# Kernel tuning notes

Measured on AMD Instinct MI355X. Metric: run time of the kernel, lower is better.

The kernel has to match this reference:

```python
import jax, jax.numpy as jnp
import numpy as np

B, T, D = 1, 1024, 2048
F_DIM = 1408
E = 8
TOPK = 2


def setup_inputs() -> dict:
    key = jax.random.key(0)
    ks = jax.random.split(key, 5)
    x = jax.random.normal(ks[0], (B, T, D), dtype=jnp.float32)
    # torch nn.Linear weight layout: [out_features, in_features]
    gate_w = jax.random.normal(ks[1], (E, D), dtype=jnp.float32) * 0.02
    gate_proj = jax.random.normal(ks[2], (E, F_DIM, D), dtype=jnp.float32) * 0.02
    up_proj = jax.random.normal(ks[3], (E, F_DIM, D), dtype=jnp.float32) * 0.02
    down_proj = jax.random.normal(ks[4], (E, D, F_DIM), dtype=jnp.float32) * 0.02
    return {"x": x, "gate_w": gate_w, "gate_proj": gate_proj,
            "up_proj": up_proj, "down_proj": down_proj}


def reference(x, gate_w, gate_proj, up_proj, down_proj):
    b, t, d = x.shape
    x_flat = x.reshape(-1, d)                                  # [N, D]
    n = x_flat.shape[0]
    # Router: top-k logits then softmax over the selected k.
    router_logits = x_flat @ gate_w.T                          # [N, E]
    top_w, sel = jax.lax.top_k(router_logits, TOPK)            # [N, K]
    top_w = jax.nn.softmax(top_w, axis=-1)                     # [N, K]
    # Scatter routing weights into dense per-token expert weights [N, E].
    tok_ids = jnp.arange(n)[:, None]
    tw = jnp.zeros((n, E), dtype=x.dtype).at[tok_ids, sel].add(top_w)
    # Dense expert compute (mathematically identical: unselected experts get
    # zero combine weight). SwiGLU per expert.
    g = jnp.einsum('nd,efd->enf', x_flat, gate_proj)           # [E, N, F]
    u = jnp.einsum('nd,efd->enf', x_flat, up_proj)             # [E, N, F]
    h = jax.nn.silu(g) * u                                     # [E, N, F]
    eo = jnp.einsum('enf,edf->end', h, down_proj)              # [E, N, D]
    out = jnp.einsum('end,ne->nd', eo, tw)                     # [N, D]
    return out.reshape(b, t, d)
```

## Files before the change

kernel.cpp:

```cpp
#include <hip/hip_runtime.h>
#include <hip/hip_bf16.h>
#include <stdint.h>

typedef __attribute__((ext_vector_type(8))) short short8;
typedef __attribute__((ext_vector_type(4))) float f32x4;
typedef unsigned int u32;
typedef unsigned short u16;

static constexpr int N_TOK = 1024;
static constexpr int DDIM = 2048;
static constexpr int FDIM = 1408;
static constexpr int NEXP = 8;
static constexpr int MAXROWS = 3072;
static constexpr int NT128 = 24;

static constexpr size_t O_META   = 0;
static constexpr size_t O_TE128  = 256;
static constexpr size_t O_TR128  = 384;
static constexpr size_t O_ROWTOK = 768;
static constexpr size_t O_TOKROWS= O_ROWTOK + (size_t)MAXROWS * 4;
static constexpr size_t O_SEL    = O_TOKROWS + 2048 * 4;
static constexpr size_t O_W      = O_SEL + 2048 * 4;
static constexpr size_t O_XBF    = (O_W + 2048 * 4 + 255) & ~(size_t)255;
static constexpr size_t O_H      = O_XBF + (size_t)(N_TOK + 1) * DDIM * 2;
static constexpr size_t O_EO     = O_H + (size_t)MAXROWS * FDIM * 2;

static __device__ __forceinline__ u16 f2bf(float f) {
    return __builtin_bit_cast(u16, __float2bfloat16(f));
}
static __device__ __forceinline__ float bf2f(u16 s) {
    u32 u = ((u32)s) << 16;
    return __builtin_bit_cast(float, u);
}
static __device__ __forceinline__ u32 pack2(float a, float b) {
    return (u32)f2bf(a) | ((u32)f2bf(b) << 16);
}
static __device__ __forceinline__ void gload16(const void* g, void* l) {
    __builtin_amdgcn_global_load_lds(
        (const __attribute__((address_space(1))) void*)g,
        (__attribute__((address_space(3))) void*)l, 16, 0, 0);
}
#define PIN() __builtin_amdgcn_sched_barrier(0)
static __device__ __forceinline__ void sync_lgkm() {
    asm volatile("s_waitcnt lgkmcnt(0)" ::: "memory");
    __builtin_amdgcn_s_barrier();
    __builtin_amdgcn_sched_barrier(0);
}

__global__ __launch_bounds__(256) void xcast_kernel(
    const float* __restrict__ x, u16* __restrict__ xbf)
{
    const long idx = ((long)blockIdx.x * 256 + threadIdx.x) * 8;
    uint4 v = {0u, 0u, 0u, 0u};
    if (idx < (long)N_TOK * DDIM) {
        const float4 f0 = *(const float4*)(x + idx);
        const float4 f1 = *(const float4*)(x + idx + 4);
        v.x = pack2(f0.x, f0.y); v.y = pack2(f0.z, f0.w);
        v.z = pack2(f1.x, f1.y); v.w = pack2(f1.z, f1.w);
    }
    *(uint4*)(xbf + idx) = v;
}

__global__ __launch_bounds__(256) void router_kernel(
    const float* __restrict__ x, const float* __restrict__ gw,
    int* __restrict__ sel, float* __restrict__ wout)
{
    __shared__ float xs[DDIM];
    __shared__ float lg[NEXP];
    const int tok = blockIdx.x;
    const float* xr = x + (size_t)tok * DDIM;
    for (int i = threadIdx.x; i < DDIM / 4; i += 256)
        ((float4*)xs)[i] = ((const float4*)xr)[i];
    __syncthreads();
    const int wid = threadIdx.x >> 6, lane = threadIdx.x & 63;
    for (int i = 0; i < 2; i++) {
        const int e = wid * 2 + i;
        const float* g = gw + (size_t)e * DDIM;
        float s = 0.f;
        for (int k = lane; k < DDIM; k += 64) s += xs[k] * g[k];
        for (int off = 32; off > 0; off >>= 1) s += __shfl_down(s, off);
        if (lane == 0) lg[e] = s;
    }
    __syncthreads();
    if (threadIdx.x == 0) {
        int i1 = 0;
        for (int e = 1; e < NEXP; e++) if (lg[e] > lg[i1]) i1 = e;
        int i2 = -1;
        for (int e = 0; e < NEXP; e++) {
            if (e == i1) continue;
            if (i2 < 0 || lg[e] > lg[i2]) i2 = e;
        }
        const float e2 = __expf(lg[i2] - lg[i1]);
        const float w1 = 1.f / (1.f + e2);
        sel[tok * 2] = i1; sel[tok * 2 + 1] = i2;
        wout[tok * 2] = w1; wout[tok * 2 + 1] = e2 * w1;
    }
}

__global__ __launch_bounds__(512) void build_kernel(
    const int* __restrict__ sel,
    int* __restrict__ meta, int* __restrict__ te128, int* __restrict__ tr128,
    int* __restrict__ row_tok, int* __restrict__ tok_rows)
{
    __shared__ int s0[N_TOK], s1[N_TOK];
    __shared__ u16 p0[N_TOK], p1[N_TOK];
    __shared__ int counts[NEXP], offs[NEXP];
    for (int i = threadIdx.x; i < N_TOK; i += 512) {
        s0[i] = sel[i * 2]; s1[i] = sel[i * 2 + 1];
    }
    __syncthreads();
    const int e = threadIdx.x >> 6, lane = threadIdx.x & 63;
    int base = 0;
    for (int c = 0; c < N_TOK / 64; c++) {
        const int tk = c * 64 + lane;
        const int slot = (s0[tk] == e) ? 0 : ((s1[tk] == e) ? 1 : -1);
        const unsigned long long m = __ballot(slot >= 0);
        const int pre = __popcll(m & ((1ull << lane) - 1ull));
        if (slot == 0) p0[tk] = (u16)(base + pre);
        else if (slot == 1) p1[tk] = (u16)(base + pre);
        base += __popcll(m);
    }
    if (lane == 0) counts[e] = base;
    __syncthreads();
    if (threadIdx.x == 0) {
        int off = 0, n128 = 0;
        for (int qq = 0; qq < NEXP; qq++) {
            offs[qq] = off;
            const int pc = (counts[qq] + 127) & ~127;
            for (int i = 0; i < pc / 128; i++) { te128[n128] = qq; tr128[n128] = off + i * 128; n128++; }
            off += pc;
        }
        meta[0] = n128; meta[1] = off;
    }
    __syncthreads();
    const int off = offs[e];
    for (int c = 0; c < N_TOK / 64; c++) {
        const int tk = c * 64 + lane;
        const int slot = (s0[tk] == e) ? 0 : ((s1[tk] == e) ? 1 : -1);
        if (slot >= 0) {
            const int row = off + (slot ? p1[tk] : p0[tk]);
            row_tok[row] = tk;
            tok_rows[tk * 2 + slot] = row;
        }
    }
    const int cnt = counts[e];
    const int pc = (cnt + 127) & ~127;
    for (int p = cnt + lane; p < pc; p += 64) row_tok[off + p] = -1;
}

__global__ __launch_bounds__(512, 4) void mlp1_kernel(
    const u16* __restrict__ xbf,
    const float* __restrict__ gp, const float* __restrict__ upw,
    u16* __restrict__ h,
    const int* __restrict__ meta, const int* __restrict__ te128,
    const int* __restrict__ tr128, const int* __restrict__ row_tok)
{
    const int tile = blockIdx.y;
    const int nb = blockIdx.x;
    if (tile >= meta[0]) return;
    const int n0 = nb * 32;
    const int e = te128[tile];
    const int r0g = tr128[tile];

    __shared__ __align__(16) u16 As[2][128 * 64];
    __shared__ __align__(16) u16 Bs0[2][32 * 64];
    __shared__ __align__(16) u16 Bs1[2][32 * 64];

    const int t = threadIdx.x;
    const int wid = t >> 6, lane = t & 63;
    const int lr = lane & 15, lhi = lane >> 4;

    const u16* asrc[2];
    int aldsoff[2];
    #pragma unroll
    for (int j = 0; j < 2; j++) {
        const int row = wid * 16 + j * 8 + (lane >> 3);
        const int gran = (lane & 7) ^ (row & 7);
        const int tok = row_tok[r0g + row];
        asrc[j] = xbf + (size_t)(tok < 0 ? N_TOK : tok) * DDIM + gran * 8;
        aldsoff[j] = (wid * 2 + j) * 512;
    }

    const int rb = t >> 4, c4 = t & 15;
    const float* brow0 = gp  + (size_t)e * FDIM * DDIM + (size_t)(n0 + rb) * DDIM + c4 * 4;
    const float* brow1 = upw + (size_t)e * FDIM * DDIM + (size_t)(n0 + rb) * DDIM + c4 * 4;
    const int sOffB = rb * 64 + (((c4 >> 1) ^ (rb & 7)) * 8) + (c4 & 1) * 4;

    const int wm = wid * 16;

    f32x4 acc0[2], acc1[2];
    acc0[0] = acc0[1] = acc1[0] = acc1[1] = f32x4{0.f, 0.f, 0.f, 0.f};
    float4 pb0P, pb1P, pb0Q, pb1Q;

    auto STAGEA = [&](int bsel, int k0) {
        #pragma unroll
        for (int j = 0; j < 2; j++)
            gload16(asrc[j] + k0, &As[bsel][aldsoff[j]]);
    };
    auto LOADB_P = [&](int k0) {
        pb0P = *(const float4*)(brow0 + k0);
        pb1P = *(const float4*)(brow1 + k0);
    };
    auto LOADB_Q = [&](int k0) {
        pb0Q = *(const float4*)(brow0 + k0);
        pb1Q = *(const float4*)(brow1 + k0);
    };
    auto STOREB_P = [&](int bsel) {
        uint2 v0; v0.x = pack2(pb0P.x, pb0P.y); v0.y = pack2(pb0P.z, pb0P.w);
        *(uint2*)(&Bs0[bsel][sOffB]) = v0;
        uint2 v1; v1.x = pack2(pb1P.x, pb1P.y); v1.y = pack2(pb1P.z, pb1P.w);
        *(uint2*)(&Bs1[bsel][sOffB]) = v1;
    };
    auto STOREB_Q = [&](int bsel) {
        uint2 v0; v0.x = pack2(pb0Q.x, pb0Q.y); v0.y = pack2(pb0Q.z, pb0Q.w);
        *(uint2*)(&Bs0[bsel][sOffB]) = v0;
        uint2 v1; v1.x = pack2(pb1Q.x, pb1Q.y); v1.y = pack2(pb1Q.z, pb1Q.w);
        *(uint2*)(&Bs1[bsel][sOffB]) = v1;
    };
    auto COMPUTE = [&](int bsel) {
        __builtin_amdgcn_s_setprio(1);
        #pragma unroll
        for (int ks = 0; ks < 2; ks++) {
            short8 a, b0[2], b1[2];
            {
                const int rowa = wm + lr;
                const int gr = (ks * 4 + lhi) ^ (rowa & 7);
                a = *(const short8*)(&As[bsel][rowa * 64 + gr * 8]);
            }
            #pragma unroll
            for (int n = 0; n < 2; n++) {
                const int rowb = n * 16 + lr;
                const int gr = (ks * 4 + lhi) ^ (rowb & 7);
                b0[n] = *(const short8*)(&Bs0[bsel][rowb * 64 + gr * 8]);
                b1[n] = *(const short8*)(&Bs1[bsel][rowb * 64 + gr * 8]);
            }
            #pragma unroll
            for (int n = 0; n < 2; n++) {
                acc0[n] = __builtin_amdgcn_mfma_f32_16x16x32_bf16(a, b0[n], acc0[n], 0, 0, 0);
                acc1[n] = __builtin_amdgcn_mfma_f32_16x16x32_bf16(a, b1[n], acc1[n], 0, 0, 0);
            }
        }
        __builtin_amdgcn_s_setprio(0);
    };

    constexpr int NT = DDIM / 64;
    STAGEA(0, 0);
    PIN();
    LOADB_P(0);
    LOADB_Q(64);
    PIN();
    STOREB_P(0);
    sync_lgkm();
    for (int kt = 0; kt < NT; kt += 2) {
        STAGEA(1, ((kt + 1) & (NT - 1)) * 64);
        PIN();
        LOADB_P(((kt + 2) & (NT - 1)) * 64);
        PIN();
        STOREB_Q(1);
        asm volatile("s_waitcnt vmcnt(4)" ::: "memory");
        PIN();
        COMPUTE(0);
        sync_lgkm();
        STAGEA(0, ((kt + 2) & (NT - 1)) * 64);
        PIN();
        LOADB_Q(((kt + 3) & (NT - 1)) * 64);
        PIN();
        STOREB_P(0);
        asm volatile("s_waitcnt vmcnt(4)" ::: "memory");
        PIN();
        COMPUTE(1);
        sync_lgkm();
    }

    #pragma unroll
    for (int n = 0; n < 2; n++) {
        const int col = n0 + n * 16 + lr;
        #pragma unroll
        for (int j = 0; j < 4; j++) {
            const int row = r0g + wm + lhi * 4 + j;
            const float g = acc0[n][j], u = acc1[n][j];
            const float hv = g / (1.f + __expf(-g)) * u;
            h[(size_t)row * FDIM + col] = f2bf(hv);
        }
    }
}

__global__ __launch_bounds__(512, 4) void down_kernel(
    const u16* __restrict__ h, const float* __restrict__ dp,
    u16* __restrict__ eo,
    const int* __restrict__ meta, const int* __restrict__ te128,
    const int* __restrict__ tr128)
{
    const int tile = blockIdx.y;
    const int nb = blockIdx.x;
    if (tile >= meta[0]) return;
    const int n0 = nb * 32;
    const int e = te128[tile];
    const int r0g = tr128[tile];

    __shared__ __align__(16) u16 As[2][128 * 64];
    __shared__ __align__(16) u16 Bs[2][32 * 64];

    const int t = threadIdx.x;
    const int wid = t >> 6, lane = t & 63;
    const int lr = lane & 15, lhi = lane >> 4;

    const u16* asrc[2];
    int aldsoff[2];
    #pragma unroll
    for (int j = 0; j < 2; j++) {
        const int row = wid * 16 + j * 8 + (lane >> 3);
        const int gran = (lane & 7) ^ (row & 7);
        asrc[j] = h + (size_t)(r0g + row) * FDIM + gran * 8;
        aldsoff[j] = (wid * 2 + j) * 512;
    }

    const int rb = t >> 4, c4 = t & 15;
    const float* brow = dp + (size_t)e * DDIM * FDIM + (size_t)(n0 + rb) * FDIM + c4 * 4;
    const int sOffB = rb * 64 + (((c4 >> 1) ^ (rb & 7)) * 8) + (c4 & 1) * 4;

    const int wm = wid * 16;

    f32x4 acc[2];
    acc[0] = acc[1] = f32x4{0.f, 0.f, 0.f, 0.f};
    float4 pbP, pbQ;

    auto STAGEA = [&](int bsel, int k0) {
        #pragma unroll
        for (int j = 0; j < 2; j++)
            gload16(asrc[j] + k0, &As[bsel][aldsoff[j]]);
    };
    auto LOADB_P = [&](int k0) { pbP = *(const float4*)(brow + k0); };
    auto LOADB_Q = [&](int k0) { pbQ = *(const float4*)(brow + k0); };
    auto STOREB_P = [&](int bsel) {
        uint2 v; v.x = pack2(pbP.x, pbP.y); v.y = pack2(pbP.z, pbP.w);
        *(uint2*)(&Bs[bsel][sOffB]) = v;
    };
    auto STOREB_Q = [&](int bsel) {
        uint2 v; v.x = pack2(pbQ.x, pbQ.y); v.y = pack2(pbQ.z, pbQ.w);
        *(uint2*)(&Bs[bsel][sOffB]) = v;
    };
    auto COMPUTE = [&](int bsel) {
        __builtin_amdgcn_s_setprio(1);
        #pragma unroll
        for (int ks = 0; ks < 2; ks++) {
            short8 a, b[2];
            {
                const int rowa = wm + lr;
                const int gr = (ks * 4 + lhi) ^ (rowa & 7);
                a = *(const short8*)(&As[bsel][rowa * 64 + gr * 8]);
            }
            #pragma unroll
            for (int n = 0; n < 2; n++) {
                const int rowb = n * 16 + lr;
                const int gr = (ks * 4 + lhi) ^ (rowb & 7);
                b[n] = *(const short8*)(&Bs[bsel][rowb * 64 + gr * 8]);
            }
            #pragma unroll
            for (int n = 0; n < 2; n++)
                acc[n] = __builtin_amdgcn_mfma_f32_16x16x32_bf16(a, b[n], acc[n], 0, 0, 0);
        }
        __builtin_amdgcn_s_setprio(0);
    };

    constexpr int NT = FDIM / 64;
    STAGEA(0, 0);
    PIN();
    LOADB_P(0);
    LOADB_Q(64);
    PIN();
    STOREB_P(0);
    sync_lgkm();
    for (int kt = 0; kt < NT; kt += 2) {
        int k1 = kt + 1; if (k1 >= NT) k1 = 0;
        int k2 = kt + 2; if (k2 >= NT) k2 = 0;
        int k3 = kt + 3; if (k3 >= NT) k3 = 0;
        STAGEA(1, k1 * 64);
        PIN();
        LOADB_P(k2 * 64);
        PIN();
        STOREB_Q(1);
        asm volatile("s_waitcnt vmcnt(3)" ::: "memory");
        PIN();
        COMPUTE(0);
        sync_lgkm();
        STAGEA(0, k2 * 64);
        PIN();
        LOADB_Q(k3 * 64);
        PIN();
        STOREB_P(0);
        asm volatile("s_waitcnt vmcnt(3)" ::: "memory");
        PIN();
        COMPUTE(1);
        sync_lgkm();
    }

    #pragma unroll
    for (int n = 0; n < 2; n++) {
        const int col = n0 + n * 16 + lr;
        #pragma unroll
        for (int j = 0; j < 4; j++) {
            const int row = r0g + wm + lhi * 4 + j;
            eo[(size_t)row * DDIM + col] = f2bf(acc[n][j]);
        }
    }
}

__global__ __launch_bounds__(256) void combine_kernel(
    const u16* __restrict__ eo, const int* __restrict__ tok_rows,
    const float* __restrict__ w, float* __restrict__ out)
{
    const int tok = blockIdx.x;
    const int r1 = tok_rows[tok * 2], r2 = tok_rows[tok * 2 + 1];
    const float w1 = w[tok * 2], w2 = w[tok * 2 + 1];
    const int d = threadIdx.x * 8;
    const uint4 a = *(const uint4*)(eo + (size_t)r1 * DDIM + d);
    const uint4 b = *(const uint4*)(eo + (size_t)r2 * DDIM + d);
    const u32 av[4] = {a.x, a.y, a.z, a.w};
    const u32 bv[4] = {b.x, b.y, b.z, b.w};
    float4 o0, o1;
    float* op[8] = {&o0.x, &o0.y, &o0.z, &o0.w, &o1.x, &o1.y, &o1.z, &o1.w};
    #pragma unroll
    for (int i = 0; i < 4; i++) {
        *op[2 * i]     = w1 * bf2f((u16)(av[i] & 0xffff)) + w2 * bf2f((u16)(bv[i] & 0xffff));
        *op[2 * i + 1] = w1 * bf2f((u16)(av[i] >> 16))    + w2 * bf2f((u16)(bv[i] >> 16));
    }
    float4* po = (float4*)(out + (size_t)tok * DDIM + d);
    po[0] = o0; po[1] = o1;
}

extern "C" void kernel_launch(void* const* d_in, const int* in_sizes, int n_in,
                              void* d_out, int out_size, void* d_ws, size_t ws_size,
                              hipStream_t stream) {
    const float* x  = (const float*)d_in[0];
    const float* gw = (const float*)d_in[1];
    const float* gp = (const float*)d_in[2];
    const float* up = (const float*)d_in[3];
    const float* dp = (const float*)d_in[4];
    float* out = (float*)d_out;
    char* ws = (char*)d_ws;

    int*   meta     = (int*)(ws + O_META);
    int*   te128    = (int*)(ws + O_TE128);
    int*   tr128    = (int*)(ws + O_TR128);
    int*   row_tok  = (int*)(ws + O_ROWTOK);
    int*   tok_rows = (int*)(ws + O_TOKROWS);
    int*   sel      = (int*)(ws + O_SEL);
    float* w        = (float*)(ws + O_W);
    u16*   xbf      = (u16*)(ws + O_XBF);
    u16*   h        = (u16*)(ws + O_H);
    u16*   eo       = (u16*)(ws + O_EO);

    xcast_kernel<<<((N_TOK + 1) * DDIM) / (256 * 8), 256, 0, stream>>>(x, xbf);
    router_kernel<<<N_TOK, 256, 0, stream>>>(x, gw, sel, w);
    build_kernel<<<1, 512, 0, stream>>>(sel, meta, te128, tr128, row_tok, tok_rows);
    mlp1_kernel<<<dim3(FDIM / 32, NT128), 512, 0, stream>>>(
        xbf, gp, up, h, meta, te128, tr128, row_tok);
    down_kernel<<<dim3(DDIM / 32, NT128), 512, 0, stream>>>(
        h, dp, eo, meta, te128, tr128);
    combine_kernel<<<N_TOK, 256, 0, stream>>>(eo, tok_rows, w, out);
}
```

Measured before the change: 178.5 us.

## Fuse combine into down-proj via routing-weighted h and atomic scatter-add

Routing weights are folded into the SwiGLU output in mlp1, and down_kernel scatters results with float atomicAdd directly into a pre-zeroed output. This removes the bf16 expert-output buffer and the separate combine kernel. The x-to-bf16 cast moves into the router kernel, and down_kernel's N tile grows from 32 to 64 columns with wider B loads. The cost is atomic contention on the output, an extra zeroing pass, and bf16 rounding of the weighted h values.

Result: slower. 184.5 us (+3.4%).

```diff
diff --git a/kernel.cpp b/kernel.cpp
--- a/kernel.cpp
+++ b/kernel.cpp
@@ -23,7 +23,7 @@
 static constexpr size_t O_W      = O_SEL + 2048 * 4;
 static constexpr size_t O_XBF    = (O_W + 2048 * 4 + 255) & ~(size_t)255;
 static constexpr size_t O_H      = O_XBF + (size_t)(N_TOK + 1) * DDIM * 2;
-static constexpr size_t O_EO     = O_H + (size_t)MAXROWS * FDIM * 2;
+static constexpr size_t O_WROW   = O_H + (size_t)MAXROWS * FDIM * 2;
 
 static __device__ __forceinline__ u16 f2bf(float f) {
     return __builtin_bit_cast(u16, __float2bfloat16(f));
@@ -47,23 +47,15 @@
     __builtin_amdgcn_sched_barrier(0);
 }
 
-__global__ __launch_bounds__(256) void xcast_kernel(
-    const float* __restrict__ x, u16* __restrict__ xbf)
+__global__ __launch_bounds__(256) void zero_out_kernel(float* __restrict__ out)
 {
-    const long idx = ((long)blockIdx.x * 256 + threadIdx.x) * 8;
-    uint4 v = {0u, 0u, 0u, 0u};
-    if (idx < (long)N_TOK * DDIM) {
-        const float4 f0 = *(const float4*)(x + idx);
-        const float4 f1 = *(const float4*)(x + idx + 4);
-        v.x = pack2(f0.x, f0.y); v.y = pack2(f0.z, f0.w);
-        v.z = pack2(f1.x, f1.y); v.w = pack2(f1.z, f1.w);
-    }
-    *(uint4*)(xbf + idx) = v;
+    const long idx = ((long)blockIdx.x * 256 + threadIdx.x) * 4;
+    *(float4*)(out + idx) = make_float4(0.f, 0.f, 0.f, 0.f);
 }
 
 __global__ __launch_bounds__(256) void router_kernel(
     const float* __restrict__ x, const float* __restrict__ gw,
-    int* __restrict__ sel, float* __restrict__ wout)
+    int* __restrict__ sel, float* __restrict__ wout, u16* __restrict__ xbf)
 {
     __shared__ float xs[DDIM];
     __shared__ float lg[NEXP];
@@ -72,6 +64,15 @@
     for (int i = threadIdx.x; i < DDIM / 4; i += 256)
         ((float4*)xs)[i] = ((const float4*)xr)[i];
     __syncthreads();
+    {
+        const int i = threadIdx.x * 8;
+        uint4 v;
+        v.x = pack2(xs[i], xs[i + 1]);     v.y = pack2(xs[i + 2], xs[i + 3]);
+        v.z = pack2(xs[i + 4], xs[i + 5]); v.w = pack2(xs[i + 6], xs[i + 7]);
+        *(uint4*)(xbf + (size_t)tok * DDIM + i) = v;
+        if (tok == 0)
+            *(uint4*)(xbf + (size_t)N_TOK * DDIM + i) = uint4{0u, 0u, 0u, 0u};
+    }
     const int wid = threadIdx.x >> 6, lane = threadIdx.x & 63;
     for (int i = 0; i < 2; i++) {
         const int e = wid * 2 + i;
@@ -98,9 +99,9 @@
 }
 
 __global__ __launch_bounds__(512) void build_kernel(
-    const int* __restrict__ sel,
+    const int* __restrict__ sel, const float* __restrict__ w,
     int* __restrict__ meta, int* __restrict__ te128, int* __restrict__ tr128,
-    int* __restrict__ row_tok, int* __restrict__ tok_rows)
+    int* __restrict__ row_tok, int* __restrict__ tok_rows, float* __restrict__ wrow)
 {
     __shared__ int s0[N_TOK], s1[N_TOK];
     __shared__ u16 p0[N_TOK], p1[N_TOK];
@@ -141,11 +142,12 @@
             const int row = off + (slot ? p1[tk] : p0[tk]);
             row_tok[row] = tk;
             tok_rows[tk * 2 + slot] = row;
+            wrow[row] = w[tk * 2 + slot];
         }
     }
     const int cnt = counts[e];
     const int pc = (cnt + 127) & ~127;
-    for (int p = cnt + lane; p < pc; p += 64) row_tok[off + p] = -1;
+    for (int p = cnt + lane; p < pc; p += 64) { row_tok[off + p] = -1; wrow[off + p] = 0.f; }
 }
 
 __global__ __launch_bounds__(512, 4) void mlp1_kernel(
@@ -153,7 +155,8 @@
     const float* __restrict__ gp, const float* __restrict__ upw,
     u16* __restrict__ h,
     const int* __restrict__ meta, const int* __restrict__ te128,
-    const int* __restrict__ tr128, const int* __restrict__ row_tok)
+    const int* __restrict__ tr128, const int* __restrict__ row_tok,
+    const float* __restrict__ wrow)
 {
     const int tile = blockIdx.y;
     const int nb = blockIdx.x;
@@ -273,33 +276,34 @@
     }
 
     #pragma unroll
-    for (int n = 0; n < 2; n++) {
-        const int col = n0 + n * 16 + lr;
+    for (int j = 0; j < 4; j++) {
+        const int row = r0g + wm + lhi * 4 + j;
+        const float wr = wrow[row];
         #pragma unroll
-        for (int j = 0; j < 4; j++) {
-            const int row = r0g + wm + lhi * 4 + j;
+        for (int n = 0; n < 2; n++) {
+            const int col = n0 + n * 16 + lr;
             const float g = acc0[n][j], u = acc1[n][j];
-            const float hv = g / (1.f + __expf(-g)) * u;
+            const float hv = g / (1.f + __expf(-g)) * u * wr;
             h[(size_t)row * FDIM + col] = f2bf(hv);
         }
     }
 }
 
-__global__ __launch_bounds__(512, 4) void down_kernel(
+__global__ __launch_bounds__(512, 6) void down_kernel(
     const u16* __restrict__ h, const float* __restrict__ dp,
-    u16* __restrict__ eo,
+    float* __restrict__ out,
     const int* __restrict__ meta, const int* __restrict__ te128,
-    const int* __restrict__ tr128)
+    const int* __restrict__ tr128, const int* __restrict__ row_tok)
 {
     const int tile = blockIdx.y;
     const int nb = blockIdx.x;
     if (tile >= meta[0]) return;
-    const int n0 = nb * 32;
+    const int n0 = nb * 64;
     const int e = te128[tile];
     const int r0g = tr128[tile];
 
     __shared__ __align__(16) u16 As[2][128 * 64];
-    __shared__ __align__(16) u16 Bs[2][32 * 64];
+    __shared__ __align__(16) u16 Bs[2][64 * 64];
 
     const int t = threadIdx.x;
     const int wid = t >> 6, lane = t & 63;
@@ -315,50 +319,55 @@
         aldsoff[j] = (wid * 2 + j) * 512;
     }
 
-    const int rb = t >> 4, c4 = t & 15;
-    const float* brow = dp + (size_t)e * DDIM * FDIM + (size_t)(n0 + rb) * FDIM + c4 * 4;
-    const int sOffB = rb * 64 + (((c4 >> 1) ^ (rb & 7)) * 8) + (c4 & 1) * 4;
+    const int rb = t >> 3, g8 = t & 7;
+    const float* brow = dp + (size_t)e * DDIM * FDIM + (size_t)(n0 + rb) * FDIM + g8 * 8;
+    const int sOffB = rb * 64 + ((g8 ^ (rb & 7)) * 8);
 
     const int wm = wid * 16;
 
-    f32x4 acc[2];
-    acc[0] = acc[1] = f32x4{0.f, 0.f, 0.f, 0.f};
-    float4 pbP, pbQ;
+    f32x4 acc[4];
+    #pragma unroll
+    for (int n = 0; n < 4; n++) acc[n] = f32x4{0.f,0.f,0.f,0.f};
+    float4 paP, pbP, paQ, pbQ;
 
     auto STAGEA = [&](int bsel, int k0) {
         #pragma unroll
         for (int j = 0; j < 2; j++)
             gload16(asrc[j] + k0, &As[bsel][aldsoff[j]]);
     };
-    auto LOADB_P = [&](int k0) { pbP = *(const float4*)(brow + k0); };
-    auto LOADB_Q = [&](int k0) { pbQ = *(const float4*)(brow + k0); };
+    auto LOADB_P = [&](int k0) {
+        paP = *(const float4*)(brow + k0); pbP = *(const float4*)(brow + k0 + 4);
+    };
+    auto LOADB_Q = [&](int k0) {
+        paQ = *(const float4*)(brow + k0); pbQ = *(const float4*)(brow + k0 + 4);
+    };
     auto STOREB_P = [&](int bsel) {
-        uint2 v; v.x = pack2(pbP.x, pbP.y); v.y = pack2(pbP.z, pbP.w);
-        *(uint2*)(&Bs[bsel][sOffB]) = v;
+        uint4 v; v.x = pack2(paP.x, paP.y); v.y = pack2(paP.z, paP.w);
+        v.z = pack2(pbP.x, pbP.y); v.w = pack2(pbP.z, pbP.w);
+        *(uint4*)(&Bs[bsel][sOffB]) = v;
     };
     auto STOREB_Q = [&](int bsel) {
-        uint2 v; v.x = pack2(pbQ.x, pbQ.y); v.y = pack2(pbQ.z, pbQ.w);
-        *(uint2*)(&Bs[bsel][sOffB]) = v;
+        uint4 v; v.x = pack2(paQ.x, paQ.y); v.y = pack2(paQ.z, paQ.w);
+        v.z = pack2(pbQ.x, pbQ.y); v.w = pack2(pbQ.z, pbQ.w);
+        *(uint4*)(&Bs[bsel][sOffB]) = v;
     };
     auto COMPUTE = [&](int bsel) {
         __builtin_amdgcn_s_setprio(1);
         #pragma unroll
         for (int ks = 0; ks < 2; ks++) {
-            short8 a, b[2];
+            short8 a;
             {
                 const int rowa = wm + lr;
                 const int gr = (ks * 4 + lhi) ^ (rowa & 7);
                 a = *(const short8*)(&As[bsel][rowa * 64 + gr * 8]);
             }
             #pragma unroll
-            for (int n = 0; n < 2; n++) {
+            for (int n = 0; n < 4; n++) {
                 const int rowb = n * 16 + lr;
                 const int gr = (ks * 4 + lhi) ^ (rowb & 7);
-                b[n] = *(const short8*)(&Bs[bsel][rowb * 64 + gr * 8]);
-            }
-            #pragma unroll
-            for (int n = 0; n < 2; n++)
-                acc[n] = __builtin_amdgcn_mfma_f32_16x16x32_bf16(a, b[n], acc[n], 0, 0, 0);
+                const short8 b = *(const short8*)(&Bs[bsel][rowb * 64 + gr * 8]);
+                acc[n] = __builtin_amdgcn_mfma_f32_16x16x32_bf16(a, b, acc[n], 0, 0, 0);
+            }
         }
         __builtin_amdgcn_s_setprio(0);
     };
@@ -380,7 +389,7 @@
         LOADB_P(k2 * 64);
         PIN();
         STOREB_Q(1);
-        asm volatile("s_waitcnt vmcnt(3)" ::: "memory");
+        asm volatile("s_waitcnt vmcnt(4)" ::: "memory");
         PIN();
         COMPUTE(0);
         sync_lgkm();
@@ -389,44 +398,25 @@
         LOADB_Q(k3 * 64);
         PIN();
         STOREB_P(0);
-        asm volatile("s_waitcnt vmcnt(3)" ::: "memory");
+        asm volatile("s_waitcnt vmcnt(4)" ::: "memory");
         PIN();
         COMPUTE(1);
         sync_lgkm();
     }
 
     #pragma unroll
-    for (int n = 0; n < 2; n++) {
-        const int col = n0 + n * 16 + lr;
-        #pragma unroll
-        for (int j = 0; j < 4; j++) {
-            const int row = r0g + wm + lhi * 4 + j;
-            eo[(size_t)row * DDIM + col] = f2bf(acc[n][j]);
-        }
-    }
-}
-
-__global__ __launch_bounds__(256) void combine_kernel(
-    const u16* __restrict__ eo, const int* __restrict__ tok_rows,
-    const float* __restrict__ w, float* __restrict__ out)
-{
-    const int tok = blockIdx.x;
-    const int r1 = tok_rows[tok * 2], r2 = tok_rows[tok * 2 + 1];
-    const float w1 = w[tok * 2], w2 = w[tok * 2 + 1];
-    const int d = threadIdx.x * 8;
-    const uint4 a = *(const uint4*)(eo + (size_t)r1 * DDIM + d);
-    const uint4 b = *(const uint4*)(eo + (size_t)r2 * DDIM + d);
-    const u32 av[4] = {a.x, a.y, a.z, a.w};
-    const u32 bv[4] = {b.x, b.y, b.z, b.w};
-    float4 o0, o1;
-    float* op[8] = {&o0.x, &o0.y, &o0.z, &o0.w, &o1.x, &o1.y, &o1.z, &o1.w};
-    #pragma unroll
-    for (int i = 0; i < 4; i++) {
-        *op[2 * i]     = w1 * bf2f((u16)(av[i] & 0xffff)) + w2 * bf2f((u16)(bv[i] & 0xffff));
-        *op[2 * i + 1] = w1 * bf2f((u16)(av[i] >> 16))    + w2 * bf2f((u16)(bv[i] >> 16));
-    }
-    float4* po = (float4*)(out + (size_t)tok * DDIM + d);
-    po[0] = o0; po[1] = o1;
+    for (int j = 0; j < 4; j++) {
+        const int row = r0g + wm + lhi * 4 + j;
+        const int tok = row_tok[row];
+        if (tok >= 0) {
+            float* orow = out + (size_t)tok * DDIM;
+            #pragma unroll
+            for (int n = 0; n < 4; n++) {
+                const int col = n0 + n * 16 + lr;
+                atomicAdd(orow + col, acc[n][j]);
+            }
+        }
+    }
 }
 
 extern "C" void kernel_launch(void* const* d_in, const int* in_sizes, int n_in,
@@ -449,14 +439,14 @@
     float* w        = (float*)(ws + O_W);
     u16*   xbf      = (u16*)(ws + O_XBF);
     u16*   h        = (u16*)(ws + O_H);
-    u16*   eo       = (u16*)(ws + O_EO);
-
-    xcast_kernel<<<((N_TOK + 1) * DDIM) / (256 * 8), 256, 0, stream>>>(x, xbf);
-    router_kernel<<<N_TOK, 256, 0, stream>>>(x, gw, sel, w);
-    build_kernel<<<1, 512, 0, stream>>>(sel, meta, te128, tr128, row_tok, tok_rows);
+    float* wrow     = (float*)(ws + O_WROW);
+
+    zero_out_kernel<<<(N_TOK * DDIM) / (256 * 4), 256, 0, stream>>>(out);
+    router_kernel<<<N_TOK, 256, 0, stream>>>(x, gw, sel, w, xbf);
+    build_kernel<<<1, 512, 0, stream>>>(sel, w, meta, te128, tr128,
+                                        row_tok, tok_rows, wrow);
     mlp1_kernel<<<dim3(FDIM / 32, NT128), 512, 0, stream>>>(
-        xbf, gp, up, h, meta, te128, tr128, row_tok);
-    down_kernel<<<dim3(DDIM / 32, NT128), 512, 0, stream>>>(
-        h, dp, eo, meta, te128, tr128);
-    combine_kernel<<<N_TOK, 256, 0, stream>>>(eo, tok_rows, w, out);
-}
+        xbf, gp, up, h, meta, te128, tr128, row_tok, wrow);
+    down_kernel<<<dim3(DDIM / 64, NT128), 512, 0, stream>>>(
+        h, dp, out, meta, te128, tr128, row_tok);
+}
```
